# Kernel optimization log

Hardware: AMD Instinct MI355X
Metric: run time of the kernel (lower is better)

The kernel has to match this reference:

```python
import jax, jax.numpy as jnp
import numpy as np

B, Q, HIST, HID, NH, D, BS, NBLK, NUMB = 8, 512, 1536, 4096, 32, 128, 64, 32, 256


def _rope(x, pos):
    # GPT-NeoX-style rotary used by Falcon: rotate_half over full head_dim.
    Dh = x.shape[-1]
    inv = 1.0 / (10000.0 ** (jnp.arange(0, Dh, 2, dtype=jnp.float32) / Dh))  # [D/2]
    ang = pos.astype(jnp.float32)[:, None] * inv[None, :]                    # [T, D/2]
    cos = jnp.concatenate([jnp.cos(ang), jnp.cos(ang)], -1)[None, :, None, :]
    sin = jnp.concatenate([jnp.sin(ang), jnp.sin(ang)], -1)[None, :, None, :]
    half = Dh // 2
    rot = jnp.concatenate([-x[..., half:], x[..., :half]], -1)
    return x * cos + rot * sin


def setup_inputs() -> dict:
    key = jax.random.key(0)
    ks = jax.random.split(key, 6)
    hidden_states = jax.random.normal(ks[0], (1, B * Q, HID), jnp.float32) * 0.02
    qkv_weight = jax.random.normal(ks[1], ((NH + 2) * D, HID), jnp.float32) * 0.02
    dense_weight = jax.random.normal(ks[2], (HID, NH * D), jnp.float32) * 0.02
    past_key = jax.random.normal(ks[3], (NUMB, BS, 1, D), jnp.float32) * 0.02
    past_value = jax.random.normal(ks[4], (NUMB, BS, 1, D), jnp.float32) * 0.02
    q_start_loc = (jnp.arange(B) * Q).astype(jnp.int32)
    q_seq_length = jnp.full((B,), Q, jnp.int32)
    history_lengths = jnp.full((B,), HIST, jnp.int32)
    # each sequence owns NBLK distinct cache blocks (shuffled block table)
    block_offsets = jax.random.permutation(ks[5], NUMB).reshape(B, NBLK).astype(jnp.int32)
    position_ids_1d = (history_lengths[:, None] + jnp.arange(Q, dtype=jnp.int32)[None, :]).reshape(-1)
    return dict(hidden_states=hidden_states, qkv_weight=qkv_weight, dense_weight=dense_weight,
                past_key=past_key, past_value=past_value, q_start_loc=q_start_loc,
                q_seq_length=q_seq_length, history_lengths=history_lengths,
                block_offsets=block_offsets, position_ids_1d=position_ids_1d)


def reference(hidden_states, qkv_weight, dense_weight, past_key, past_value,
              q_start_loc, q_seq_length, history_lengths, block_offsets, position_ids_1d):
    T = hidden_states.shape[1]
    Bn = block_offsets.shape[0]
    Qn = T // Bn
    Dh = past_key.shape[-1]
    BSz = past_key.shape[1]
    # fused QKV projection
    fused = hidden_states @ qkv_weight.T                      # [1, T, (NH+2)*D]
    NHh = fused.shape[-1] // Dh - 2
    qkv = fused.reshape(1, T, NHh + 2, Dh)
    q = qkv[:, :, :NHh]                                       # [1, T, NH, D]
    k = qkv[:, :, NHh:NHh + 1]                                 # [1, T, 1, D]
    v = qkv[:, :, NHh + 1:]                                    # [1, T, 1, D]
    # inline rotary embedding on q, k
    q = _rope(q, position_ids_1d)
    k = _rope(k, position_ids_1d)
    # fill_kv_cache: scatter new K/V into paged cache via block table
    seq_id = jnp.repeat(jnp.arange(Bn), Qn)                   # [T]
    pos = position_ids_1d.astype(jnp.int32)                   # absolute kv position
    blk = block_offsets[seq_id, pos // BSz]                   # [T] physical block id
    off = pos % BSz
    past_key = past_key.at[blk, off].set(k.reshape(T, 1, Dh))
    past_value = past_value.at[blk, off].set(v.reshape(T, 1, Dh))
    # paged_attention_fwd: gather per-sequence K/V from paged cache
    KVc = block_offsets.shape[1] * BSz                        # kv capacity == kv_len here
    kseq = past_key[block_offsets].reshape(Bn, KVc, Dh)       # [B, KV, D] (1 kv head squeezed)
    vseq = past_value[block_offsets].reshape(Bn, KVc, Dh)
    qb = q.reshape(Bn, Qn, NHh, Dh)
    scale = 1.0 / jnp.sqrt(jnp.float32(Dh))
    scores = jnp.einsum('bqhd,bkd->bhqk', qb, kseq) * scale   # [B, H, Q, KV]
    qpos = history_lengths[:, None] + jnp.arange(Qn)[None, :] # [B, Q]
    mask = jnp.arange(KVc)[None, None, :] <= qpos[:, :, None] # causal + length mask
    scores = jnp.where(mask[:, None, :, :], scores, jnp.float32(-1e30))
    attn = jax.nn.softmax(scores, axis=-1)
    out = jnp.einsum('bhqk,bkd->bqhd', attn, vseq)            # [B, Q, H, D]
    out = out.reshape(1, T, NHh * Dh)
    return out @ dense_weight.T                                # [1, T, hidden]
```

## Files before the change

kernel.cpp:

```cpp
#include <hip/hip_runtime.h>

typedef __attribute__((ext_vector_type(8))) short bf16x8;
typedef __attribute__((ext_vector_type(4))) float f32x4;
typedef __attribute__((ext_vector_type(16))) float f32x16;
typedef __attribute__((ext_vector_type(2))) unsigned int u32x2;

constexpr int B_ = 8, Q_ = 512, HIST_ = 1536, HID_ = 4096, NH_ = 32, D_ = 128;
constexpr int BS_ = 64, NBLK_ = 32;
constexpr int T_ = B_ * Q_;
constexpr int QKVN = (NH_ + 2) * D_;
constexpr int KVC = NBLK_ * BS_;

__device__ __forceinline__ unsigned short f2bf(float f) {
  union { float f; unsigned u; } v; v.f = f;
  unsigned r = v.u + 0x7FFFu + ((v.u >> 16) & 1u);
  return (unsigned short)(r >> 16);
}
__device__ __forceinline__ float bf2f(unsigned short s) {
  union { unsigned u; float f; } v; v.u = ((unsigned)s) << 16;
  return v.f;
}
__device__ __forceinline__ int cvtpk_bf16(float lo, float hi) {
  int r;
  asm("v_cvt_pk_bf16_f32 %0, %1, %2" : "=v"(r) : "v"(lo), "v"(hi));
  return r;
}

__global__ void k_conv(const float* __restrict__ in, unsigned short* __restrict__ out, int n4) {
  int i = blockIdx.x * blockDim.x + threadIdx.x;
  int stride = gridDim.x * blockDim.x;
  for (; i < n4; i += stride) {
    float4 v = reinterpret_cast<const float4*>(in)[i];
    ushort4 o;
    o.x = f2bf(v.x); o.y = f2bf(v.y); o.z = f2bf(v.z); o.w = f2bf(v.w);
    reinterpret_cast<ushort4*>(out)[i] = o;
  }
}

#define LDA4(af, cur_, qq)                                                              \
  {                                                                                     \
    const unsigned short* a_t = sA + (cur_) * 16384;                                    \
    const int r0 = wr * 128 + (qq) * 32 + lr;                                           \
    const int r1 = r0 + 16;                                                             \
    af[0][0] = *(const bf16x8*)&a_t[r0 * 64 + ((lk ^ (r0 & 7)) << 3)];                  \
    af[0][1] = *(const bf16x8*)&a_t[r0 * 64 + (((4 + lk) ^ (r0 & 7)) << 3)];            \
    af[1][0] = *(const bf16x8*)&a_t[r1 * 64 + ((lk ^ (r1 & 7)) << 3)];                  \
    af[1][1] = *(const bf16x8*)&a_t[r1 * 64 + (((4 + lk) ^ (r1 & 7)) << 3)];            \
  }

#define LDB2(dst, cur_, nn)                                                             \
  {                                                                                     \
    const unsigned short* b_t = sB + (cur_) * 16384;                                    \
    const int rb = wc * 64 + (nn) * 16 + lr;                                            \
    dst[nn][0] = *(const bf16x8*)&b_t[rb * 64 + ((lk ^ (rb & 7)) << 3)];                \
    dst[nn][1] = *(const bf16x8*)&b_t[rb * 64 + (((4 + lk) ^ (rb & 7)) << 3)];          \
  }

#define MFMA16(qq, af, Bf)                                                              \
  __builtin_amdgcn_s_setprio(1);                                                        \
  acc[(qq)*2+0][0] = __builtin_amdgcn_mfma_f32_16x16x32_bf16(af[0][0], Bf[0][0], acc[(qq)*2+0][0], 0, 0, 0); \
  acc[(qq)*2+0][1] = __builtin_amdgcn_mfma_f32_16x16x32_bf16(af[0][0], Bf[1][0], acc[(qq)*2+0][1], 0, 0, 0); \
  acc[(qq)*2+0][2] = __builtin_amdgcn_mfma_f32_16x16x32_bf16(af[0][0], Bf[2][0], acc[(qq)*2+0][2], 0, 0, 0); \
  acc[(qq)*2+0][3] = __builtin_amdgcn_mfma_f32_16x16x32_bf16(af[0][0], Bf[3][0], acc[(qq)*2+0][3], 0, 0, 0); \
  acc[(qq)*2+1][0] = __builtin_amdgcn_mfma_f32_16x16x32_bf16(af[1][0], Bf[0][0], acc[(qq)*2+1][0], 0, 0, 0); \
  acc[(qq)*2+1][1] = __builtin_amdgcn_mfma_f32_16x16x32_bf16(af[1][0], Bf[1][0], acc[(qq)*2+1][1], 0, 0, 0); \
  acc[(qq)*2+1][2] = __builtin_amdgcn_mfma_f32_16x16x32_bf16(af[1][0], Bf[2][0], acc[(qq)*2+1][2], 0, 0, 0); \
  acc[(qq)*2+1][3] = __builtin_amdgcn_mfma_f32_16x16x32_bf16(af[1][0], Bf[3][0], acc[(qq)*2+1][3], 0, 0, 0); \
  acc[(qq)*2+0][0] = __builtin_amdgcn_mfma_f32_16x16x32_bf16(af[0][1], Bf[0][1], acc[(qq)*2+0][0], 0, 0, 0); \
  acc[(qq)*2+0][1] = __builtin_amdgcn_mfma_f32_16x16x32_bf16(af[0][1], Bf[1][1], acc[(qq)*2+0][1], 0, 0, 0); \
  acc[(qq)*2+0][2] = __builtin_amdgcn_mfma_f32_16x16x32_bf16(af[0][1], Bf[2][1], acc[(qq)*2+0][2], 0, 0, 0); \
  acc[(qq)*2+0][3] = __builtin_amdgcn_mfma_f32_16x16x32_bf16(af[0][1], Bf[3][1], acc[(qq)*2+0][3], 0, 0, 0); \
  acc[(qq)*2+1][0] = __builtin_amdgcn_mfma_f32_16x16x32_bf16(af[1][1], Bf[0][1], acc[(qq)*2+1][0], 0, 0, 0); \
  acc[(qq)*2+1][1] = __builtin_amdgcn_mfma_f32_16x16x32_bf16(af[1][1], Bf[1][1], acc[(qq)*2+1][1], 0, 0, 0); \
  acc[(qq)*2+1][2] = __builtin_amdgcn_mfma_f32_16x16x32_bf16(af[1][1], Bf[2][1], acc[(qq)*2+1][2], 0, 0, 0); \
  acc[(qq)*2+1][3] = __builtin_amdgcn_mfma_f32_16x16x32_bf16(af[1][1], Bf[3][1], acc[(qq)*2+1][3], 0, 0, 0); \
  __builtin_amdgcn_s_setprio(0);

#define SYNCPT                                                                          \
  asm volatile("s_waitcnt vmcnt(4)" ::: "memory");                                      \
  __builtin_amdgcn_s_barrier();                                                         \
  asm volatile("" ::: "memory");

#define TILE(t_, cur_, BCUR, BNEXT)                                                     \
  {                                                                                     \
    bf16x8 af[2][2];                                                                    \
                         \
    LDA4(af, cur_, 0);                                                                  \
    stage(A, m0, sA, (t_) + 1, 0);                                                      \
    MFMA16(0, af, BCUR);                                                                \
    LDA4(af, cur_, 1);                                                                  \
    stage(A, m0, sA, (t_) + 1, 1);                                                      \
    MFMA16(1, af, BCUR);                                                                \
    SYNCPT;                                             \
                              \
    LDA4(af, cur_, 2);                                                                  \
    LDB2(BNEXT, (cur_) ^ 1, 0); LDB2(BNEXT, (cur_) ^ 1, 1);                             \
    stage(Bm, n0, sB, (t_) + 2, 0);                                                     \
    MFMA16(2, af, BCUR);                                                                \
    LDA4(af, cur_, 3);                                                                  \
    LDB2(BNEXT, (cur_) ^ 1, 2); LDB2(BNEXT, (cur_) ^ 1, 3);                             \
    stage(Bm, n0, sB, (t_) + 2, 1);                                                     \
    MFMA16(3, af, BCUR);                                                                \
    SYNCPT;                                             \
  }

__global__ __launch_bounds__(512, 2) void k_gemm256(const unsigned short* __restrict__ A,
                          const unsigned short* __restrict__ Bm,
                          float* __restrict__ Cf, unsigned short* __restrict__ Cb,
                          int MB, int K, int ldc) {
  extern __shared__ unsigned short smem[];
  unsigned short* sA = smem;
  unsigned short* sB = smem + 32768;
  const int tid = threadIdx.x, lane = tid & 63, w = tid >> 6;
  const int wr = w >> 2, wc = w & 3;
  const int lr = lane & 15, lk = lane >> 4;

  const int nwg = gridDim.x, orig = blockIdx.x;
  const int q8 = nwg >> 3, r8 = nwg & 7, xcd = orig & 7;
  const int wg = (xcd < r8 ? xcd * (q8 + 1) : r8 * (q8 + 1) + (xcd - r8) * q8) + (orig >> 3);
  const int m0 = (wg % MB) * 256;
  const int n0 = (wg / MB) * 256;
  const int NT = K >> 6;

  f32x4 acc[8][4];
#pragma unroll
  for (int mf = 0; mf < 8; ++mf)
#pragma unroll
    for (int nf = 0; nf < 4; ++nf) acc[mf][nf] = f32x4{0.f, 0.f, 0.f, 0.f};

  auto stage = [&](const unsigned short* __restrict__ Mat, int rbase, unsigned short* regionBase,
                   int ts, int half) {
    const int di = ts < NT ? ts : NT - 1;
    const size_t k0 = (size_t)di << 6;
    char* hb = (char*)(regionBase + (ts & 1) * 16384 + half * 8192);
#pragma unroll
    for (int c = 0; c < 2; ++c) {
      const int ob = c * 8192 + (w << 10) + (lane << 4);
      const int row = ob >> 7;
      const int sl = ((ob >> 4) & 7) ^ (row & 7);
      const unsigned short* src = Mat + (size_t)(rbase + half * 128 + row) * K + k0 + sl * 8;
      __builtin_amdgcn_global_load_lds((const __attribute__((address_space(1))) void*)src,
          (__attribute__((address_space(3))) void*)(hb + c * 8192 + (w << 10)), 16, 0, 0);
    }
  };

  stage(A, m0, sA, 0, 0); stage(A, m0, sA, 0, 1);
  stage(Bm, n0, sB, 0, 0); stage(Bm, n0, sB, 0, 1);
  stage(Bm, n0, sB, 1, 0); stage(Bm, n0, sB, 1, 1);
  asm volatile("s_waitcnt vmcnt(4)" ::: "memory");
  __builtin_amdgcn_s_barrier();
  asm volatile("" ::: "memory");
  bf16x8 bX[4][2], bY[4][2];
  LDB2(bX, 0, 0); LDB2(bX, 0, 1); LDB2(bX, 0, 2); LDB2(bX, 0, 3);

  for (int t = 0; t < NT; t += 2) {
    TILE(t, 0, bX, bY)
    TILE(t + 1, 1, bY, bX)
  }
  asm volatile("s_waitcnt vmcnt(0)" ::: "memory");

#pragma unroll
  for (int mf = 0; mf < 8; ++mf)
#pragma unroll
    for (int nf = 0; nf < 4; ++nf)
#pragma unroll
      for (int j = 0; j < 4; ++j) {
        const int rr = m0 + wr * 128 + mf * 16 + lk * 4 + j;
        const int cc = n0 + wc * 64 + nf * 16 + lr;
        if (Cb) Cb[(size_t)rr * ldc + cc] = f2bf(acc[mf][nf][j]);
        else Cf[(size_t)rr * ldc + cc] = acc[mf][nf][j];
      }
}

__global__ void k_rope(const unsigned short* __restrict__ fused,
                       const int* __restrict__ pos_ids,
                       unsigned short* __restrict__ qb,
                       unsigned short* __restrict__ kseq,
                       unsigned short* __restrict__ vtg) {
  int t = blockIdx.x;
  int d = threadIdx.x;
  int b = t >> 9, q = t & 511;
  int pos = pos_ids[t];
  __shared__ float cs[64], sn[64];
  if (d < 64) {
    float inv = powf(10000.f, -(float)d * (1.f / 64.f));
    float ang = (float)pos * inv;
    cs[d] = cosf(ang);
    sn[d] = sinf(ang);
  }
  __syncthreads();
  const float scale = 0.1275174313836907f;
  float c = cs[d & 63], s = sn[d & 63];
  const unsigned short* row = fused + (size_t)t * QKVN;
#pragma unroll 4
  for (int h = 0; h < NH_; ++h) {
    float x = bf2f(row[h * D_ + d]);
    float xr = (d < 64) ? -bf2f(row[h * D_ + d + 64]) : bf2f(row[h * D_ + d - 64]);
    qb[(((size_t)(b * NH_ + h)) * Q_ + q) * D_ + d] = f2bf((x * c + xr * s) * scale);
  }
  {
    float x = bf2f(row[NH_ * D_ + d]);
    float xr = (d < 64) ? -bf2f(row[NH_ * D_ + d + 64]) : bf2f(row[NH_ * D_ + d - 64]);
    kseq[((size_t)b * KVC + pos) * D_ + d] = f2bf(x * c + xr * s);
  }
  vtg[((size_t)b * D_ + d) * KVC + pos] = row[(NH_ + 1) * D_ + d];
}

__global__ void k_gather(const float* __restrict__ pk, const float* __restrict__ pv,
                         const int* __restrict__ bo,
                         unsigned short* __restrict__ kseq, unsigned short* __restrict__ vtg) {
  __shared__ unsigned short vl[64 * 140];
  const int ptile = blockIdx.x;
  const int b = ptile / (HIST_ / 64);
  const int p0 = (ptile % (HIST_ / 64)) * 64;
  const int tid = threadIdx.x;
  const int blk = bo[b * NBLK_ + (p0 >> 6)];
#pragma unroll
  for (int c = 0; c < 8; ++c) {
    int u = c * 256 + tid;
    int p = u >> 5, d4 = u & 31;
    size_t src = ((size_t)blk * BS_ + p) * D_ + d4 * 4;
    float4 kv = *reinterpret_cast<const float4*>(pk + src);
    ushort4 ko;
    ko.x = f2bf(kv.x); ko.y = f2bf(kv.y); ko.z = f2bf(kv.z); ko.w = f2bf(kv.w);
    *reinterpret_cast<ushort4*>(kseq + ((size_t)b * KVC + p0 + p) * D_ + d4 * 4) = ko;
    float4 vv = *reinterpret_cast<const float4*>(pv + src);
    ushort4 vo;
    vo.x = f2bf(vv.x); vo.y = f2bf(vv.y); vo.z = f2bf(vv.z); vo.w = f2bf(vv.w);
    *reinterpret_cast<ushort4*>(&vl[p * 140 + d4 * 4]) = vo;
  }
  __syncthreads();
#pragma unroll
  for (int c = 0; c < 4; ++c) {
    int u = c * 256 + tid;
    int d = u >> 3, pg = u & 7;
    bf16x8 vv8;
#pragma unroll
    for (int i = 0; i < 8; ++i) vv8[i] = (short)vl[(pg * 8 + i) * 140 + d];
    *reinterpret_cast<bf16x8*>(vtg + ((size_t)b * D_ + d) * KVC + p0 + pg * 8) = vv8;
  }
}

__global__ __launch_bounds__(512, 2) void k_attn(const unsigned short* __restrict__ qb,
                       const unsigned short* __restrict__ kseq,
                       const unsigned short* __restrict__ vtg,
                       const int* __restrict__ histL,
                       unsigned short* __restrict__ outb) {
  __shared__ alignas(16) unsigned short kl[2][64 * 128];
  __shared__ alignas(16) unsigned short vt[2][128 * 64];
  const int qt = blockIdx.x, hp = blockIdx.y, b = blockIdx.z;
  const int tid = threadIdx.x, lane = tid & 63, w = tid >> 6;
  const int H = lane >> 5, q = lane & 31;
  const int h = hp * 8 + w;
  const int q0 = qt * 32;
  const int hist = histL[b];
  const unsigned short* kseq_b = kseq + (size_t)b * KVC * D_;
  const unsigned short* vtg_b  = vtg + (size_t)b * D_ * KVC;

  const unsigned short* qrow = qb + (((size_t)(b * NH_ + h)) * Q_ + q0 + q) * D_;
  bf16x8 aq[8];
#pragma unroll
  for (int ds = 0; ds < 8; ++ds)
    aq[ds] = *reinterpret_cast<const bf16x8*>(qrow + ds * 16 + H * 8);

  f32x16 o[4];
#pragma unroll
  for (int db = 0; db < 4; ++db)
#pragma unroll
    for (int r = 0; r < 16; ++r) o[db][r] = 0.f;
  float m = -1e30f, l = 0.f;

  const int ntiles = (hist + q0 + 32 + 63) >> 6;

  auto STAGE = [&](int bufi, int kv0) {
#pragma unroll
    for (int c = 0; c < 2; ++c) {
      int ob = c * 8192 + tid * 16;
      int row = ob >> 8;
      int sp = (ob >> 4) & 15;
      const unsigned short* src = kseq_b + (size_t)(kv0 + row) * D_ + (((sp ^ (row & 15)) << 3));
      __builtin_amdgcn_global_load_lds((const __attribute__((address_space(1))) void*)src,
          (__attribute__((address_space(3))) void*)(&kl[bufi][c * 4096 + w * 512]), 16, 0, 0);
    }
#pragma unroll
    for (int c = 0; c < 2; ++c) {
      int ob = c * 8192 + tid * 16;
      int row = ob >> 7;
      int sp = (ob >> 4) & 7;
      const unsigned short* src = vtg_b + (size_t)row * KVC + kv0 + (((sp ^ (row & 7)) << 3));
      __builtin_amdgcn_global_load_lds((const __attribute__((address_space(1))) void*)src,
          (__attribute__((address_space(3))) void*)(&vt[bufi][c * 4096 + w * 512]), 16, 0, 0);
    }
  };

  STAGE(0, 0);
  __syncthreads();

  for (int it = 0; it < ntiles; ++it) {
    const int cur = it & 1;
    if (it + 1 < ntiles) STAGE(cur ^ 1, (it + 1) * 64);
    const unsigned short* kb = kl[cur];
    const unsigned short* vb = vt[cur];

    f32x16 sa = f32x16{0.f,0.f,0.f,0.f,0.f,0.f,0.f,0.f,0.f,0.f,0.f,0.f,0.f,0.f,0.f,0.f};
    f32x16 sb = sa, sc = sa, sd = sa;
#pragma unroll
    for (int ds = 0; ds < 4; ++ds) {
      const int sl = ((2 * ds + H) ^ (q & 15)) << 3;
      bf16x8 k0 = *reinterpret_cast<const bf16x8*>(kb + q * 128 + sl);
      bf16x8 k1 = *reinterpret_cast<const bf16x8*>(kb + (32 + q) * 128 + sl);
      sa = __builtin_amdgcn_mfma_f32_32x32x16_bf16(k0, aq[ds], sa, 0, 0, 0);
      sc = __builtin_amdgcn_mfma_f32_32x32x16_bf16(k1, aq[ds], sc, 0, 0, 0);
    }
#pragma unroll
    for (int ds = 4; ds < 8; ++ds) {
      const int sl = ((2 * ds + H) ^ (q & 15)) << 3;
      bf16x8 k0 = *reinterpret_cast<const bf16x8*>(kb + q * 128 + sl);
      bf16x8 k1 = *reinterpret_cast<const bf16x8*>(kb + (32 + q) * 128 + sl);
      sb = __builtin_amdgcn_mfma_f32_32x32x16_bf16(k0, aq[ds], sb, 0, 0, 0);
      sd = __builtin_amdgcn_mfma_f32_32x32x16_bf16(k1, aq[ds], sd, 0, 0, 0);
    }
    f32x16 s0 = sa + sb;
    f32x16 s1 = sc + sd;

    if (it == ntiles - 1) {
      const int limit = hist + q0 + q - it * 64 - 4 * H;
#pragma unroll
      for (int r = 0; r < 16; ++r) {
        const int koff = (r & 3) + 8 * ((r >> 2) & 1) + 16 * (r >> 3);
        if (koff > limit) s0[r] = -1e30f;
        if (32 + koff > limit) s1[r] = -1e30f;
      }
    }

    float pmax = s0[0];
#pragma unroll
    for (int r = 1; r < 16; ++r) pmax = fmaxf(pmax, s0[r]);
#pragma unroll
    for (int r = 0; r < 16; ++r) pmax = fmaxf(pmax, s1[r]);
    pmax = fmaxf(pmax, __shfl_xor(pmax, 32));
    if (__any(pmax > m + 11.54f)) {
      float mn = fmaxf(m, pmax);
      float al = exp2f(m - mn);
      m = mn;
      l *= al;
#pragma unroll
      for (int db = 0; db < 4; ++db)
#pragma unroll
        for (int r = 0; r < 16; ++r) o[db][r] *= al;
    }
    float rs = 0.f;
#pragma unroll
    for (int r = 0; r < 16; ++r) { s0[r] = exp2f(s0[r] - m); rs += s0[r]; }
#pragma unroll
    for (int r = 0; r < 16; ++r) { s1[r] = exp2f(s1[r] - m); rs += s1[r]; }
    rs += __shfl_xor(rs, 32);
    l += rs;

#pragma unroll
    for (int s = 0; s < 4; ++s) {
      float p0, p1, p2, p3, p4, p5, p6, p7;
      if (s == 0)      { p0=s0[0];p1=s0[1];p2=s0[2];p3=s0[3];p4=s0[4];p5=s0[5];p6=s0[6];p7=s0[7]; }
      else if (s == 1) { p0=s0[8];p1=s0[9];p2=s0[10];p3=s0[11];p4=s0[12];p5=s0[13];p6=s0[14];p7=s0[15]; }
      else if (s == 2) { p0=s1[0];p1=s1[1];p2=s1[2];p3=s1[3];p4=s1[4];p5=s1[5];p6=s1[6];p7=s1[7]; }
      else             { p0=s1[8];p1=s1[9];p2=s1[10];p3=s1[11];p4=s1[12];p5=s1[13];p6=s1[14];p7=s1[15]; }
      int c01 = cvtpk_bf16(p0, p1);
      int c23 = cvtpk_bf16(p2, p3);
      int c45 = cvtpk_bf16(p4, p5);
      int c67 = cvtpk_bf16(p6, p7);
      u32x2 rA = __builtin_amdgcn_permlane32_swap(c01, c45, false, false);
      u32x2 rB = __builtin_amdgcn_permlane32_swap(c23, c67, false, false);
      union { unsigned wds[4]; bf16x8 v; } uu;
      uu.wds[0] = rA[0]; uu.wds[1] = rB[0]; uu.wds[2] = rA[1]; uu.wds[3] = rB[1];
#pragma unroll
      for (int db = 0; db < 4; ++db) {
        const int row = db * 32 + q;
        bf16x8 vf = *reinterpret_cast<const bf16x8*>(vb + row * 64 + ((((2 * s + H) ^ (row & 7))) << 3));
        o[db] = __builtin_amdgcn_mfma_f32_32x32x16_bf16(vf, uu.v, o[db], 0, 0, 0);
      }
    }
    __syncthreads();
  }

  const float il = 1.f / l;
  unsigned short* orow = outb + (size_t)(b * Q_ + q0 + q) * (NH_ * D_) + h * D_;
#pragma unroll
  for (int db = 0; db < 4; ++db)
#pragma unroll
    for (int rr = 0; rr < 4; ++rr) {
      ushort4 st;
      st.x = f2bf(o[db][rr * 4 + 0] * il);
      st.y = f2bf(o[db][rr * 4 + 1] * il);
      st.z = f2bf(o[db][rr * 4 + 2] * il);
      st.w = f2bf(o[db][rr * 4 + 3] * il);
      *reinterpret_cast<ushort4*>(orow + db * 32 + rr * 8 + 4 * H) = st;
    }
}

extern "C" void kernel_launch(void* const* d_in, const int* in_sizes, int n_in,
                              void* d_out, int out_size, void* d_ws, size_t ws_size,
                              hipStream_t stream) {
  const float* hidden = (const float*)d_in[0];
  const float* qkvw   = (const float*)d_in[1];
  const float* densew = (const float*)d_in[2];
  const float* pk     = (const float*)d_in[3];
  const float* pv     = (const float*)d_in[4];
  const int* histL    = (const int*)d_in[7];
  const int* bo       = (const int*)d_in[8];
  const int* posids   = (const int*)d_in[9];
  float* out = (float*)d_out;

  char* ws = (char*)d_ws;
  unsigned short* ws_hidden = (unsigned short*)(ws);
  unsigned short* ws_w      = (unsigned short*)(ws + 33554432);
  unsigned short* ws_fused  = (unsigned short*)(ws + 69206016);
  unsigned short* ws_q      = (unsigned short*)(ws + 104857600);
  unsigned short* ws_k      = (unsigned short*)(ws + 138412032);
  unsigned short* ws_vt     = (unsigned short*)(ws + 142606336);
  unsigned short* ws_attn   = ws_hidden;

  k_conv<<<2048, 256, 0, stream>>>(hidden, ws_hidden, T_ * HID_ / 4);
  k_conv<<<2048, 256, 0, stream>>>(qkvw, ws_w, QKVN * HID_ / 4);
  k_gemm256<<<dim3((T_ / 256) * (QKVN / 256)), 512, 131072, stream>>>(
      ws_hidden, ws_w, nullptr, ws_fused, T_ / 256, HID_, QKVN);
  k_rope<<<T_, 128, 0, stream>>>(ws_fused, posids, ws_q, ws_k, ws_vt);
  k_gather<<<B_ * (HIST_ / 64), 256, 0, stream>>>(pk, pv, bo, ws_k, ws_vt);
  dim3 ga(Q_ / 32, NH_ / 8, B_);
  k_attn<<<ga, 512, 0, stream>>>(ws_q, ws_k, ws_vt, histL, ws_attn);
  k_conv<<<2048, 256, 0, stream>>>(densew, ws_w, HID_ * HID_ / 4);
  k_gemm256<<<dim3((T_ / 256) * (HID_ / 256)), 512, 131072, stream>>>(
      ws_attn, ws_w, out, nullptr, T_ / 256, HID_, HID_);
}
```

Before: 549.0 us.

## Fuse fp32-to-bf16 weight conversion into GEMM B-tile loading and tree-reduce softmax

Removes the two standalone weight conversion kernels by having the GEMM load fp32 weight tiles into registers, convert them to bf16 and write them swizzled into LDS. The GEMM pipeline is restructured from the two-tile interleaved schedule with partial vmcnt waits into a simpler one-tile loop that waits on all loads and syncs once per K step. Each weight tile is now read and converted once per workgroup that uses it, instead of once overall, and the simpler schedule may overlap loads and MFMA less. Separately, the attention softmax max and sum reductions become balanced trees to shorten the dependency chains.

```diff
diff --git a/kernel.cpp b/kernel.cpp
--- a/kernel.cpp
+++ b/kernel.cpp
@@ -76,36 +76,8 @@
   acc[(qq)*2+1][3] = __builtin_amdgcn_mfma_f32_16x16x32_bf16(af[1][1], Bf[3][1], acc[(qq)*2+1][3], 0, 0, 0); \
   __builtin_amdgcn_s_setprio(0);
 
-#define SYNCPT                                                                          \
-  asm volatile("s_waitcnt vmcnt(4)" ::: "memory");                                      \
-  __builtin_amdgcn_s_barrier();                                                         \
-  asm volatile("" ::: "memory");
-
-#define TILE(t_, cur_, BCUR, BNEXT)                                                     \
-  {                                                                                     \
-    bf16x8 af[2][2];                                                                    \
-                         \
-    LDA4(af, cur_, 0);                                                                  \
-    stage(A, m0, sA, (t_) + 1, 0);                                                      \
-    MFMA16(0, af, BCUR);                                                                \
-    LDA4(af, cur_, 1);                                                                  \
-    stage(A, m0, sA, (t_) + 1, 1);                                                      \
-    MFMA16(1, af, BCUR);                                                                \
-    SYNCPT;                                             \
-                              \
-    LDA4(af, cur_, 2);                                                                  \
-    LDB2(BNEXT, (cur_) ^ 1, 0); LDB2(BNEXT, (cur_) ^ 1, 1);                             \
-    stage(Bm, n0, sB, (t_) + 2, 0);                                                     \
-    MFMA16(2, af, BCUR);                                                                \
-    LDA4(af, cur_, 3);                                                                  \
-    LDB2(BNEXT, (cur_) ^ 1, 2); LDB2(BNEXT, (cur_) ^ 1, 3);                             \
-    stage(Bm, n0, sB, (t_) + 2, 1);                                                     \
-    MFMA16(3, af, BCUR);                                                                \
-    SYNCPT;                                             \
-  }
-
-__global__ __launch_bounds__(512, 2) void k_gemm256(const unsigned short* __restrict__ A,
-                          const unsigned short* __restrict__ Bm,
+__global__ __launch_bounds__(512, 2) void k_gemm(const unsigned short* __restrict__ A,
+                          const float* __restrict__ Bf,
                           float* __restrict__ Cf, unsigned short* __restrict__ Cb,
                           int MB, int K, int ldc) {
   extern __shared__ unsigned short smem[];
@@ -128,36 +100,83 @@
 #pragma unroll
     for (int nf = 0; nf < 4; ++nf) acc[mf][nf] = f32x4{0.f, 0.f, 0.f, 0.f};
 
-  auto stage = [&](const unsigned short* __restrict__ Mat, int rbase, unsigned short* regionBase,
-                   int ts, int half) {
+  auto stageA = [&](int ts) {
     const int di = ts < NT ? ts : NT - 1;
     const size_t k0 = (size_t)di << 6;
-    char* hb = (char*)(regionBase + (ts & 1) * 16384 + half * 8192);
-#pragma unroll
-    for (int c = 0; c < 2; ++c) {
-      const int ob = c * 8192 + (w << 10) + (lane << 4);
-      const int row = ob >> 7;
-      const int sl = ((ob >> 4) & 7) ^ (row & 7);
-      const unsigned short* src = Mat + (size_t)(rbase + half * 128 + row) * K + k0 + sl * 8;
-      __builtin_amdgcn_global_load_lds((const __attribute__((address_space(1))) void*)src,
-          (__attribute__((address_space(3))) void*)(hb + c * 8192 + (w << 10)), 16, 0, 0);
-    }
+    char* hb = (char*)(sA + (ts & 1) * 16384);
+#pragma unroll
+    for (int h = 0; h < 2; ++h)
+#pragma unroll
+      for (int c = 0; c < 2; ++c) {
+        const int ob = c * 8192 + (w << 10) + (lane << 4);
+        const int row = ob >> 7;
+        const int sl = ((ob >> 4) & 7) ^ (row & 7);
+        const unsigned short* src = A + (size_t)(m0 + h * 128 + row) * K + k0 + sl * 8;
+        __builtin_amdgcn_global_load_lds((const __attribute__((address_space(1))) void*)src,
+            (__attribute__((address_space(3))) void*)(hb + h * 16384 + c * 8192 + (w << 10)), 16, 0, 0);
+      }
   };
 
-  stage(A, m0, sA, 0, 0); stage(A, m0, sA, 0, 1);
-  stage(Bm, n0, sB, 0, 0); stage(Bm, n0, sB, 0, 1);
-  stage(Bm, n0, sB, 1, 0); stage(Bm, n0, sB, 1, 1);
-  asm volatile("s_waitcnt vmcnt(4)" ::: "memory");
+  float4 rB[8];
+  auto loadB = [&](int ts) {
+    const int di = ts < NT ? ts : NT - 1;
+    const int k0 = di << 6;
+#pragma unroll
+    for (int h = 0; h < 2; ++h)
+#pragma unroll
+      for (int c = 0; c < 4; ++c) {
+        const int row = h * 128 + (tid >> 2);
+        const int kp = (tid & 3) * 16 + c * 4;
+        rB[h * 4 + c] = *reinterpret_cast<const float4*>(Bf + (size_t)(n0 + row) * K + k0 + kp);
+      }
+  };
+  auto writeB = [&](int ts) {
+    unsigned short* bb = sB + (ts & 1) * 16384;
+    const int rowl = tid >> 2;
+#pragma unroll
+    for (int h = 0; h < 2; ++h) {
+      const int row = h * 128 + rowl;
+#pragma unroll
+      for (int p = 0; p < 2; ++p) {
+        const int s = (tid & 3) * 2 + p;
+        union { int wds[4]; bf16x8 v; } uu;
+        uu.wds[0] = cvtpk_bf16(rB[h * 4 + p * 2].x, rB[h * 4 + p * 2].y);
+        uu.wds[1] = cvtpk_bf16(rB[h * 4 + p * 2].z, rB[h * 4 + p * 2].w);
+        uu.wds[2] = cvtpk_bf16(rB[h * 4 + p * 2 + 1].x, rB[h * 4 + p * 2 + 1].y);
+        uu.wds[3] = cvtpk_bf16(rB[h * 4 + p * 2 + 1].z, rB[h * 4 + p * 2 + 1].w);
+        *reinterpret_cast<bf16x8*>(&bb[row * 64 + ((s ^ (row & 7)) << 3)]) = uu.v;
+      }
+    }
+  };
+
+  stageA(0);
+  loadB(0);
+  asm volatile("s_waitcnt vmcnt(0)" ::: "memory");
+  writeB(0);
+  asm volatile("s_waitcnt lgkmcnt(0)" ::: "memory");
   __builtin_amdgcn_s_barrier();
   asm volatile("" ::: "memory");
-  bf16x8 bX[4][2], bY[4][2];
-  LDB2(bX, 0, 0); LDB2(bX, 0, 1); LDB2(bX, 0, 2); LDB2(bX, 0, 3);
-
-  for (int t = 0; t < NT; t += 2) {
-    TILE(t, 0, bX, bY)
-    TILE(t + 1, 1, bY, bX)
-  }
-  asm volatile("s_waitcnt vmcnt(0)" ::: "memory");
+
+  int cur = 0;
+  for (int t = 0; t < NT; ++t) {
+    stageA(t + 1);
+    loadB(t + 1);
+    bf16x8 bfr[4][2];
+    LDB2(bfr, cur, 0); LDB2(bfr, cur, 1); LDB2(bfr, cur, 2); LDB2(bfr, cur, 3);
+    {
+      bf16x8 af[2][2];
+      LDA4(af, cur, 0); MFMA16(0, af, bfr);
+      LDA4(af, cur, 1); MFMA16(1, af, bfr);
+      LDA4(af, cur, 2); MFMA16(2, af, bfr);
+      LDA4(af, cur, 3); MFMA16(3, af, bfr);
+    }
+    asm volatile("s_waitcnt vmcnt(0)" ::: "memory");
+    writeB(t + 1);
+    asm volatile("s_waitcnt lgkmcnt(0)" ::: "memory");
+    __builtin_amdgcn_s_barrier();
+    asm volatile("" ::: "memory");
+    cur ^= 1;
+  }
 
 #pragma unroll
   for (int mf = 0; mf < 8; ++mf)
@@ -333,11 +352,12 @@
       }
     }
 
-    float pmax = s0[0];
-#pragma unroll
-    for (int r = 1; r < 16; ++r) pmax = fmaxf(pmax, s0[r]);
-#pragma unroll
-    for (int r = 0; r < 16; ++r) pmax = fmaxf(pmax, s1[r]);
+    float px[8];
+#pragma unroll
+    for (int j = 0; j < 8; ++j)
+      px[j] = fmaxf(fmaxf(s0[2 * j], s0[2 * j + 1]), fmaxf(s1[2 * j], s1[2 * j + 1]));
+    float pmax = fmaxf(fmaxf(fmaxf(px[0], px[1]), fmaxf(px[2], px[3])),
+                       fmaxf(fmaxf(px[4], px[5]), fmaxf(px[6], px[7])));
     pmax = fmaxf(pmax, __shfl_xor(pmax, 32));
     if (__any(pmax > m + 11.54f)) {
       float mn = fmaxf(m, pmax);
@@ -349,11 +369,15 @@
 #pragma unroll
         for (int r = 0; r < 16; ++r) o[db][r] *= al;
     }
-    float rs = 0.f;
-#pragma unroll
-    for (int r = 0; r < 16; ++r) { s0[r] = exp2f(s0[r] - m); rs += s0[r]; }
-#pragma unroll
-    for (int r = 0; r < 16; ++r) { s1[r] = exp2f(s1[r] - m); rs += s1[r]; }
+#pragma unroll
+    for (int r = 0; r < 16; ++r) s0[r] = exp2f(s0[r] - m);
+#pragma unroll
+    for (int r = 0; r < 16; ++r) s1[r] = exp2f(s1[r] - m);
+    float rsum[8];
+#pragma unroll
+    for (int j = 0; j < 8; ++j)
+      rsum[j] = (s0[2 * j] + s0[2 * j + 1]) + (s1[2 * j] + s1[2 * j + 1]);
+    float rs = ((rsum[0] + rsum[1]) + (rsum[2] + rsum[3])) + ((rsum[4] + rsum[5]) + (rsum[6] + rsum[7]));
     rs += __shfl_xor(rs, 32);
     l += rs;
 
@@ -412,22 +436,19 @@
 
   char* ws = (char*)d_ws;
   unsigned short* ws_hidden = (unsigned short*)(ws);
-  unsigned short* ws_w      = (unsigned short*)(ws + 33554432);
-  unsigned short* ws_fused  = (unsigned short*)(ws + 69206016);
-  unsigned short* ws_q      = (unsigned short*)(ws + 104857600);
-  unsigned short* ws_k      = (unsigned short*)(ws + 138412032);
-  unsigned short* ws_vt     = (unsigned short*)(ws + 142606336);
+  unsigned short* ws_fused  = (unsigned short*)(ws + 33554432);
+  unsigned short* ws_q      = (unsigned short*)(ws + 69206016);
+  unsigned short* ws_k      = (unsigned short*)(ws + 102760448);
+  unsigned short* ws_vt     = (unsigned short*)(ws + 106954752);
   unsigned short* ws_attn   = ws_hidden;
 
   k_conv<<<2048, 256, 0, stream>>>(hidden, ws_hidden, T_ * HID_ / 4);
-  k_conv<<<2048, 256, 0, stream>>>(qkvw, ws_w, QKVN * HID_ / 4);
-  k_gemm256<<<dim3((T_ / 256) * (QKVN / 256)), 512, 131072, stream>>>(
-      ws_hidden, ws_w, nullptr, ws_fused, T_ / 256, HID_, QKVN);
+  k_gemm<<<dim3((T_ / 256) * (QKVN / 256)), 512, 131072, stream>>>(
+      ws_hidden, qkvw, nullptr, ws_fused, T_ / 256, HID_, QKVN);
   k_rope<<<T_, 128, 0, stream>>>(ws_fused, posids, ws_q, ws_k, ws_vt);
   k_gather<<<B_ * (HIST_ / 64), 256, 0, stream>>>(pk, pv, bo, ws_k, ws_vt);
   dim3 ga(Q_ / 32, NH_ / 8, B_);
   k_attn<<<ga, 512, 0, stream>>>(ws_q, ws_k, ws_vt, histL, ws_attn);
-  k_conv<<<2048, 256, 0, stream>>>(densew, ws_w, HID_ * HID_ / 4);
-  k_gemm256<<<dim3((T_ / 256) * (HID_ / 256)), 512, 131072, stream>>>(
-      ws_attn, ws_w, out, nullptr, T_ / 256, HID_, HID_);
-}
+  k_gemm<<<dim3((T_ / 256) * (HID_ / 256)), 512, 131072, stream>>>(
+      ws_attn, densew, out, nullptr, T_ / 256, HID_, HID_);
+}
```

Result: slower. 660.1 us (+20.2%).

## Fuse RoPE and KV scatter into QKV GEMM epilogue, merge conversion kernels

Applied to the files above, without the earlier changes.

The QKV GEMM epilogue now stages the bf16 tile through LDS transposed and applies rotary embedding, Q scaling, K scatter and V-transpose scatter directly. This removes the separate fused-QKV buffer round trip and the k_rope launch. The three fp32-to-bf16 conversions are merged into one launch, and the softmax max/sum reductions in attention are rebalanced into trees. The epilogue computes sin/cos per element per block, and the V-transpose store is strided and uncoalesced, which could cost time in the epilogue.

```diff
diff --git a/kernel.cpp b/kernel.cpp
--- a/kernel.cpp
+++ b/kernel.cpp
@@ -26,14 +26,21 @@
   return r;
 }
 
-__global__ void k_conv(const float* __restrict__ in, unsigned short* __restrict__ out, int n4) {
+__global__ void k_conv3(const float* __restrict__ a, unsigned short* __restrict__ oa, int na,
+                        const float* __restrict__ b2, unsigned short* __restrict__ ob, int nb,
+                        const float* __restrict__ c3, unsigned short* __restrict__ oc, int nc) {
   int i = blockIdx.x * blockDim.x + threadIdx.x;
-  int stride = gridDim.x * blockDim.x;
-  for (; i < n4; i += stride) {
-    float4 v = reinterpret_cast<const float4*>(in)[i];
+  const int stride = gridDim.x * blockDim.x;
+  const int tot = na + nb + nc;
+  for (; i < tot; i += stride) {
+    const float* src; unsigned short* dst; int j = i;
+    if (j < na) { src = a; dst = oa; }
+    else if ((j -= na) < nb) { src = b2; dst = ob; }
+    else { j -= nb; src = c3; dst = oc; }
+    float4 v = reinterpret_cast<const float4*>(src)[j];
     ushort4 o;
     o.x = f2bf(v.x); o.y = f2bf(v.y); o.z = f2bf(v.z); o.w = f2bf(v.w);
-    reinterpret_cast<ushort4*>(out)[i] = o;
+    reinterpret_cast<ushort4*>(dst)[j] = o;
   }
 }
 
@@ -84,15 +91,13 @@
 #define TILE(t_, cur_, BCUR, BNEXT)                                                     \
   {                                                                                     \
     bf16x8 af[2][2];                                                                    \
-                         \
     LDA4(af, cur_, 0);                                                                  \
     stage(A, m0, sA, (t_) + 1, 0);                                                      \
     MFMA16(0, af, BCUR);                                                                \
     LDA4(af, cur_, 1);                                                                  \
     stage(A, m0, sA, (t_) + 1, 1);                                                      \
     MFMA16(1, af, BCUR);                                                                \
-    SYNCPT;                                             \
-                              \
+    SYNCPT;                                                                             \
     LDA4(af, cur_, 2);                                                                  \
     LDB2(BNEXT, (cur_) ^ 1, 0); LDB2(BNEXT, (cur_) ^ 1, 1);                             \
     stage(Bm, n0, sB, (t_) + 2, 0);                                                     \
@@ -101,13 +106,16 @@
     LDB2(BNEXT, (cur_) ^ 1, 2); LDB2(BNEXT, (cur_) ^ 1, 3);                             \
     stage(Bm, n0, sB, (t_) + 2, 1);                                                     \
     MFMA16(3, af, BCUR);                                                                \
-    SYNCPT;                                             \
-  }
-
-__global__ __launch_bounds__(512, 2) void k_gemm256(const unsigned short* __restrict__ A,
+    SYNCPT;                                                                             \
+  }
+
+__global__ __launch_bounds__(512, 2) void k_gemm(const unsigned short* __restrict__ A,
                           const unsigned short* __restrict__ Bm,
-                          float* __restrict__ Cf, unsigned short* __restrict__ Cb,
-                          int MB, int K, int ldc) {
+                          float* __restrict__ Cf, int MB, int K, int ldc, int mode,
+                          const int* __restrict__ posids,
+                          unsigned short* __restrict__ qb,
+                          unsigned short* __restrict__ kseq,
+                          unsigned short* __restrict__ vtg) {
   extern __shared__ unsigned short smem[];
   unsigned short* sA = smem;
   unsigned short* sB = smem + 32768;
@@ -159,51 +167,70 @@
   }
   asm volatile("s_waitcnt vmcnt(0)" ::: "memory");
 
+  if (mode == 0) {
+#pragma unroll
+    for (int mf = 0; mf < 8; ++mf)
+#pragma unroll
+      for (int nf = 0; nf < 4; ++nf)
+#pragma unroll
+        for (int j = 0; j < 4; ++j) {
+          const int rr = m0 + wr * 128 + mf * 16 + lk * 4 + j;
+          const int cc = n0 + wc * 64 + nf * 16 + lr;
+          Cf[(size_t)rr * ldc + cc] = acc[mf][nf][j];
+        }
+    return;
+  }
+
+  __builtin_amdgcn_s_barrier();
+  unsigned short* cl = smem;
 #pragma unroll
   for (int mf = 0; mf < 8; ++mf)
 #pragma unroll
-    for (int nf = 0; nf < 4; ++nf)
-#pragma unroll
-      for (int j = 0; j < 4; ++j) {
-        const int rr = m0 + wr * 128 + mf * 16 + lk * 4 + j;
-        const int cc = n0 + wc * 64 + nf * 16 + lr;
-        if (Cb) Cb[(size_t)rr * ldc + cc] = f2bf(acc[mf][nf][j]);
-        else Cf[(size_t)rr * ldc + cc] = acc[mf][nf][j];
+    for (int nf = 0; nf < 4; ++nf) {
+      const int col = wc * 64 + nf * 16 + lr;
+      const int rowb = wr * 128 + mf * 16 + lk * 4;
+      ushort4 p;
+      p.x = f2bf(acc[mf][nf][0]); p.y = f2bf(acc[mf][nf][1]);
+      p.z = f2bf(acc[mf][nf][2]); p.w = f2bf(acc[mf][nf][3]);
+      *reinterpret_cast<ushort4*>(&cl[col * 260 + rowb]) = p;
+    }
+  asm volatile("s_waitcnt lgkmcnt(0)" ::: "memory");
+  __builtin_amdgcn_s_barrier();
+
+  const int row = tid & 255;
+  const int seg = tid >> 8;
+  const int t = m0 + row;
+  const int pos = posids[t];
+  const int b = t >> 9, qq = t & 511;
+  const int head = (n0 >> 7) + seg;
+
+  if (head <= 32) {
+    const float qsc = (head < 32) ? 0.1275174313836907f : 1.0f;
+    unsigned short* dst = (head < 32)
+        ? qb + (((size_t)(b * NH_ + head)) * Q_ + qq) * D_
+        : kseq + ((size_t)b * KVC + pos) * D_;
+#pragma unroll
+    for (int g = 0; g < 8; ++g) {
+      unsigned short lo[8], hi[8];
+#pragma unroll
+      for (int u = 0; u < 8; ++u) {
+        const int dh = g * 8 + u;
+        const float x0 = bf2f(cl[(seg * 128 + dh) * 260 + row]);
+        const float x1 = bf2f(cl[(seg * 128 + dh + 64) * 260 + row]);
+        const float inv = exp2f((float)dh * -0.2076205059304451f);
+        const float ang = (float)pos * inv;
+        const float cc = cosf(ang), ss = sinf(ang);
+        lo[u] = f2bf((x0 * cc - x1 * ss) * qsc);
+        hi[u] = f2bf((x1 * cc + x0 * ss) * qsc);
       }
-}
-
-__global__ void k_rope(const unsigned short* __restrict__ fused,
-                       const int* __restrict__ pos_ids,
-                       unsigned short* __restrict__ qb,
-                       unsigned short* __restrict__ kseq,
-                       unsigned short* __restrict__ vtg) {
-  int t = blockIdx.x;
-  int d = threadIdx.x;
-  int b = t >> 9, q = t & 511;
-  int pos = pos_ids[t];
-  __shared__ float cs[64], sn[64];
-  if (d < 64) {
-    float inv = powf(10000.f, -(float)d * (1.f / 64.f));
-    float ang = (float)pos * inv;
-    cs[d] = cosf(ang);
-    sn[d] = sinf(ang);
-  }
-  __syncthreads();
-  const float scale = 0.1275174313836907f;
-  float c = cs[d & 63], s = sn[d & 63];
-  const unsigned short* row = fused + (size_t)t * QKVN;
-#pragma unroll 4
-  for (int h = 0; h < NH_; ++h) {
-    float x = bf2f(row[h * D_ + d]);
-    float xr = (d < 64) ? -bf2f(row[h * D_ + d + 64]) : bf2f(row[h * D_ + d - 64]);
-    qb[(((size_t)(b * NH_ + h)) * Q_ + q) * D_ + d] = f2bf((x * c + xr * s) * scale);
-  }
-  {
-    float x = bf2f(row[NH_ * D_ + d]);
-    float xr = (d < 64) ? -bf2f(row[NH_ * D_ + d + 64]) : bf2f(row[NH_ * D_ + d - 64]);
-    kseq[((size_t)b * KVC + pos) * D_ + d] = f2bf(x * c + xr * s);
-  }
-  vtg[((size_t)b * D_ + d) * KVC + pos] = row[(NH_ + 1) * D_ + d];
+      *reinterpret_cast<bf16x8*>(dst + g * 8) = *reinterpret_cast<bf16x8*>(lo);
+      *reinterpret_cast<bf16x8*>(dst + 64 + g * 8) = *reinterpret_cast<bf16x8*>(hi);
+    }
+  } else {
+#pragma unroll 8
+    for (int d = 0; d < 128; ++d)
+      vtg[((size_t)b * D_ + d) * KVC + pos] = cl[(128 + d) * 260 + row];
+  }
 }
 
 __global__ void k_gather(const float* __restrict__ pk, const float* __restrict__ pv,
@@ -333,11 +360,12 @@
       }
     }
 
-    float pmax = s0[0];
-#pragma unroll
-    for (int r = 1; r < 16; ++r) pmax = fmaxf(pmax, s0[r]);
-#pragma unroll
-    for (int r = 0; r < 16; ++r) pmax = fmaxf(pmax, s1[r]);
+    float px[8];
+#pragma unroll
+    for (int j = 0; j < 8; ++j)
+      px[j] = fmaxf(fmaxf(s0[2 * j], s0[2 * j + 1]), fmaxf(s1[2 * j], s1[2 * j + 1]));
+    float pmax = fmaxf(fmaxf(fmaxf(px[0], px[1]), fmaxf(px[2], px[3])),
+                       fmaxf(fmaxf(px[4], px[5]), fmaxf(px[6], px[7])));
     pmax = fmaxf(pmax, __shfl_xor(pmax, 32));
     if (__any(pmax > m + 11.54f)) {
       float mn = fmaxf(m, pmax);
@@ -349,11 +377,15 @@
 #pragma unroll
         for (int r = 0; r < 16; ++r) o[db][r] *= al;
     }
-    float rs = 0.f;
-#pragma unroll
-    for (int r = 0; r < 16; ++r) { s0[r] = exp2f(s0[r] - m); rs += s0[r]; }
-#pragma unroll
-    for (int r = 0; r < 16; ++r) { s1[r] = exp2f(s1[r] - m); rs += s1[r]; }
+#pragma unroll
+    for (int r = 0; r < 16; ++r) s0[r] = exp2f(s0[r] - m);
+#pragma unroll
+    for (int r = 0; r < 16; ++r) s1[r] = exp2f(s1[r] - m);
+    float rsum[8];
+#pragma unroll
+    for (int j = 0; j < 8; ++j)
+      rsum[j] = (s0[2 * j] + s0[2 * j + 1]) + (s1[2 * j] + s1[2 * j + 1]);
+    float rs = ((rsum[0] + rsum[1]) + (rsum[2] + rsum[3])) + ((rsum[4] + rsum[5]) + (rsum[6] + rsum[7]));
     rs += __shfl_xor(rs, 32);
     l += rs;
 
@@ -412,22 +444,21 @@
 
   char* ws = (char*)d_ws;
   unsigned short* ws_hidden = (unsigned short*)(ws);
-  unsigned short* ws_w      = (unsigned short*)(ws + 33554432);
-  unsigned short* ws_fused  = (unsigned short*)(ws + 69206016);
-  unsigned short* ws_q      = (unsigned short*)(ws + 104857600);
-  unsigned short* ws_k      = (unsigned short*)(ws + 138412032);
-  unsigned short* ws_vt     = (unsigned short*)(ws + 142606336);
+  unsigned short* ws_wq     = (unsigned short*)(ws + 33554432);
+  unsigned short* ws_wd     = (unsigned short*)(ws + 69206016);
+  unsigned short* ws_q      = (unsigned short*)(ws + 102760448);
+  unsigned short* ws_k      = (unsigned short*)(ws + 136314880);
+  unsigned short* ws_vt     = (unsigned short*)(ws + 140509184);
   unsigned short* ws_attn   = ws_hidden;
 
-  k_conv<<<2048, 256, 0, stream>>>(hidden, ws_hidden, T_ * HID_ / 4);
-  k_conv<<<2048, 256, 0, stream>>>(qkvw, ws_w, QKVN * HID_ / 4);
-  k_gemm256<<<dim3((T_ / 256) * (QKVN / 256)), 512, 131072, stream>>>(
-      ws_hidden, ws_w, nullptr, ws_fused, T_ / 256, HID_, QKVN);
-  k_rope<<<T_, 128, 0, stream>>>(ws_fused, posids, ws_q, ws_k, ws_vt);
+  k_conv3<<<2048, 256, 0, stream>>>(hidden, ws_hidden, T_ * HID_ / 4,
+                                    qkvw, ws_wq, QKVN * HID_ / 4,
+                                    densew, ws_wd, HID_ * HID_ / 4);
+  k_gemm<<<dim3((T_ / 256) * (QKVN / 256)), 512, 133120, stream>>>(
+      ws_hidden, ws_wq, nullptr, T_ / 256, HID_, 0, 1, posids, ws_q, ws_k, ws_vt);
   k_gather<<<B_ * (HIST_ / 64), 256, 0, stream>>>(pk, pv, bo, ws_k, ws_vt);
   dim3 ga(Q_ / 32, NH_ / 8, B_);
   k_attn<<<ga, 512, 0, stream>>>(ws_q, ws_k, ws_vt, histL, ws_attn);
-  k_conv<<<2048, 256, 0, stream>>>(densew, ws_w, HID_ * HID_ / 4);
-  k_gemm256<<<dim3((T_ / 256) * (HID_ / 256)), 512, 131072, stream>>>(
-      ws_attn, ws_w, out, nullptr, T_ / 256, HID_, HID_);
-}
+  k_gemm<<<dim3((T_ / 256) * (HID_ / 256)), 512, 133120, stream>>>(
+      ws_attn, ws_wd, out, T_ / 256, HID_, HID_, 0, posids, nullptr, nullptr, nullptr);
+}
```

New measurement: 557.4 us. Within noise of the previous version (+1.5%).
